# Kernel tuning notes

Measured on AMD Instinct MI355X. Metric: run time of the kernel, lower is better.

## Reference

```python
import jax, jax.numpy as jnp
import numpy as np

HIDDEN = 1024
HEADS = 16
HEAD_DIM = HIDDEN // HEADS
MAX_SEQ = 2048
BATCH = 2
SEQ = 2048


def setup_inputs() -> dict:
    key = jax.random.key(0)
    ks = jax.random.split(key, 6)
    x = jax.random.normal(ks[0], (BATCH, SEQ, HIDDEN), dtype=jnp.float32)
    # torch Linear params expressed as [in, out] weight + bias
    W1 = jax.random.normal(ks[1], (HIDDEN, 4 * HIDDEN), dtype=jnp.float32) * (HIDDEN ** -0.5)
    b1 = jnp.zeros((4 * HIDDEN,), dtype=jnp.float32)
    W2 = jax.random.normal(ks[2], (HIDDEN, HIDDEN), dtype=jnp.float32) * (HIDDEN ** -0.5)
    b2 = jnp.zeros((HIDDEN,), dtype=jnp.float32)
    rel_table = jax.random.normal(ks[3], (2 * MAX_SEQ - 1, HEADS), dtype=jnp.float32) * 0.02
    # causal mask [B, S, S]; True = keep
    attn_mask = jnp.broadcast_to(jnp.tril(jnp.ones((SEQ, SEQ), dtype=bool)), (BATCH, SEQ, SEQ))
    return {"x": x, "W1": W1, "b1": b1, "W2": W2, "b2": b2,
            "rel_table": rel_table, "attn_mask": attn_mask}


def reference(x, W1, b1, W2, b2, rel_table, attn_mask):
    B, S, H = x.shape
    # fused projection + SiLU, then chunk into U, Q, K, V
    activated = jax.nn.silu(jnp.einsum('bsh,hf->bsf', x, W1) + b1)
    U, Qp, Kp, Vp = jnp.split(activated, 4, axis=-1)
    # [B, nH, S, hd]
    def heads(t):
        return t.reshape(B, S, HEADS, HEAD_DIM).transpose(0, 2, 1, 3)
    Q, K, V = heads(Qp), heads(Kp), heads(Vp)
    scale = HEAD_DIM ** -0.5
    scores = jnp.einsum('bnqd,bnkd->bnqk', Q, K) * scale
    # relative position bias gather: idx[i,j] = i - j + MAX_SEQ - 1
    pos = jnp.arange(S)
    rel_idx = pos[:, None] - pos[None, :] + (MAX_SEQ - 1)  # [S, S]
    rel_bias = rel_table[rel_idx].transpose(2, 0, 1)[None]  # [1, nH, S, S]
    scores = scores + rel_bias
    attn = jax.nn.silu(scores)
    attn = jnp.where(attn_mask[:, None, :, :], attn, 0.0)
    out = jnp.einsum('bnqk,bnkd->bnqd', attn, V)
    out = out.transpose(0, 2, 1, 3).reshape(B, S, H)
    gated = out * U
    return jnp.einsum('bsh,hf->bsf', gated, W2) + b2
```

## Files before the change

### kernel.cpp

```cpp
#include <hip/hip_runtime.h>
#include <hip/hip_bf16.h>
#include <math.h>

#define HIDDEN   1024
#define HEADS    16
#define HEAD_DIM 64
#define SEQ      2048
#define BATCH    2
#define FDIM     4096
#define MTOT     4096
#define MAXSEQ   2048

typedef __bf16 bf16x8 __attribute__((ext_vector_type(8)));
typedef float  f32x4  __attribute__((ext_vector_type(4)));
typedef unsigned short u16;

__device__ __forceinline__ float silu_fast(float v) {
    return v * __builtin_amdgcn_rcpf(1.f + __expf(-v));
}

__device__ __forceinline__ u16 f2bf(float f) {
    union { float f; unsigned u; } v; v.f = f;
    unsigned r = v.u + 0x7FFFu + ((v.u >> 16) & 1u);
    return (u16)(r >> 16);
}
__device__ __forceinline__ float bf2f(u16 b) {
    union { unsigned u; float f; } v; v.u = ((unsigned)b) << 16;
    return v.f;
}
__device__ __forceinline__ unsigned pk2(float a, float b) {
    union { __hip_bfloat162 h; unsigned u; } z;
    z.h = __float22bfloat162_rn(make_float2(a, b));
    return z.u;
}

__device__ __forceinline__ void gload16(const void* g, void* l) {
    __builtin_amdgcn_global_load_lds(
        (const __attribute__((address_space(1))) void*)g,
        (__attribute__((address_space(3))) void*)l, 16, 0, 0);
}

__global__ __launch_bounds__(256) void prep_kernel(
    const float* __restrict__ X, const float* __restrict__ W1,
    const float* __restrict__ W2,
    u16* __restrict__ Xb, u16* __restrict__ W1t, u16* __restrict__ W2t,
    unsigned* __restrict__ ticket)
{
    __shared__ u16 T[64][72];
    const int tid = threadIdx.x;
    const int bid = blockIdx.x;

    if (bid == 0 && tid == 0) *ticket = 0u;

    if (bid < 2048) {
        int idx = (bid * 256 + tid) * 8;
        float4 a = *(const float4*)&X[idx];
        float4 b = *(const float4*)&X[idx + 4];
        uint4 pk = make_uint4(pk2(a.x, a.y), pk2(a.z, a.w),
                              pk2(b.x, b.y), pk2(b.z, b.w));
        *(uint4*)&Xb[idx] = pk;
        return;
    }

    const float* W; u16* Wt; int rows, cols, r0, c0;
    if (bid < 3072) {
        int t = bid - 2048;
        W = W1; Wt = W1t; rows = HIDDEN; cols = FDIM;
        c0 = (t & 63) * 64; r0 = (t >> 6) * 64;
    } else {
        int t = bid - 3072;
        W = W2; Wt = W2t; rows = HIDDEN; cols = HIDDEN;
        c0 = (t & 15) * 64; r0 = (t >> 4) * 64;
    }
#pragma unroll
    for (int l = 0; l < 4; ++l) {
        int idx = tid + l * 256;
        int row = idx >> 4;
        int c4  = (idx & 15) * 4;
        float4 v = *(const float4*)&W[(size_t)(r0 + row) * cols + c0 + c4];
        T[c4 + 0][row] = f2bf(v.x);
        T[c4 + 1][row] = f2bf(v.y);
        T[c4 + 2][row] = f2bf(v.z);
        T[c4 + 3][row] = f2bf(v.w);
    }
    __syncthreads();
#pragma unroll
    for (int l = 0; l < 2; ++l) {
        int idx = tid + l * 256;
        int row = idx >> 3;
        int cb  = (idx & 7) * 8;
        *(float4*)&Wt[(size_t)(c0 + row) * rows + r0 + cb] = *(float4*)&T[row][cb];
    }
}

#define GEMM_CORE(A_PTR, BT_PTR, KDIM, BM_, BN_, WMW, WNW)                     \
    enum { MTI = (BM_) / (WMW) / 16, NTI = (BN_) / (WNW) / 16,                 \
           ACH = (BM_) / 8, BCH = (BN_) / 8 };                                 \
    __shared__ __align__(16) u16 As[(BM_) * 64];                               \
    __shared__ __align__(16) u16 Bs[(BN_) * 64];                               \
    const int tid  = threadIdx.x;                                              \
    const int lane = tid & 63;                                                 \
    const int w    = tid >> 6;                                                 \
    const int wm   = w % (WMW), wn = w / (WMW);                                \
    const int l16  = lane & 15, quad = lane >> 4;                              \
    const int m0   = blockIdx.y * (BM_);                                       \
    const int n0   = blockIdx.x * (BN_);                                       \
    const int srow = lane >> 3;                                                \
    const int scol = (((lane & 7) ^ srow)) * 8;     \
    const int xr   = l16 & 7;                           \
    f32x4 acc[MTI][NTI];                                                       \
    _Pragma("unroll")                                                          \
    for (int mt = 0; mt < MTI; ++mt)                                           \
        _Pragma("unroll")                                                      \
        for (int nt = 0; nt < NTI; ++nt)                                       \
            acc[mt][nt] = (f32x4){0.f, 0.f, 0.f, 0.f};                         \
    for (int k0 = 0; k0 < (KDIM); k0 += 64) {                                  \
        __syncthreads();                                                       \
        _Pragma("unroll")                                                      \
        for (int ci = w; ci < ACH; ci += 4) {                                  \
            unsigned off = __builtin_amdgcn_readfirstlane(ci * 1024);          \
            gload16(&(A_PTR)[(size_t)(m0 + ci * 8 + srow) * (KDIM) + k0 + scol],\
                    (char*)As + off);                                          \
        }                                                                      \
        _Pragma("unroll")                                                      \
        for (int ci = w; ci < BCH; ci += 4) {                                  \
            unsigned off = __builtin_amdgcn_readfirstlane(ci * 1024);          \
            gload16(&(BT_PTR)[(size_t)(n0 + ci * 8 + srow) * (KDIM) + k0 + scol],\
                    (char*)Bs + off);                                          \
        }                                                                      \
        __syncthreads();                                                       \
        _Pragma("unroll")                                                      \
        for (int kc = 0; kc < 2; ++kc) {                                       \
            bf16x8 af[MTI], bfr[NTI];                                          \
            const int gsw = ((kc * 4 + quad) ^ xr) * 8;                        \
            _Pragma("unroll")                                                  \
            for (int t = 0; t < MTI; ++t)                                      \
                af[t]  = *(const bf16x8*)&As[(wm * (BM_ / WMW) + t * 16 + l16) \
                                             * 64 + gsw];                      \
            _Pragma("unroll")                                                  \
            for (int t = 0; t < NTI; ++t)                                      \
                bfr[t] = *(const bf16x8*)&Bs[(wn * (BN_ / WNW) + t * 16 + l16) \
                                             * 64 + gsw];                      \
            _Pragma("unroll")                                                  \
            for (int mt = 0; mt < MTI; ++mt)                                   \
                _Pragma("unroll")                                              \
                for (int nt = 0; nt < NTI; ++nt)                               \
                    acc[mt][nt] = __builtin_amdgcn_mfma_f32_16x16x32_bf16(     \
                        bfr[nt], af[mt], acc[mt][nt], 0, 0, 0);                \
        }                                                                      \
    }

__global__ __launch_bounds__(256, 1) void gemm1_mfma_kernel(
    const u16* __restrict__ A, const u16* __restrict__ Bt,
    const float* __restrict__ b1,
    u16* __restrict__ Ub, u16* __restrict__ Qh,
    u16* __restrict__ Kh, u16* __restrict__ Vh)
{
    GEMM_CORE(A, Bt, HIDDEN, 256, 128, 2, 2)

    const int chunk = n0 >> 10;
    u16* dstbase = (chunk == 0) ? Ub : (chunk == 1) ? Qh : (chunk == 2) ? Kh : Vh;
    const float postscale = (chunk == 1) ? 0.125f : 1.0f;

    float4 bias4[NTI]; int nloc[NTI];
#pragma unroll
    for (int nt = 0; nt < NTI; ++nt) {
        int nb = n0 + wn * 64 + nt * 16 + quad * 4;
        bias4[nt] = *(const float4*)&b1[nb];
        nloc[nt] = nb & 1023;
    }
#pragma unroll
    for (int mt = 0; mt < MTI; ++mt) {
        int m  = m0 + wm * 128 + mt * 16 + l16;
        int bb = m >> 11, s = m & 2047;
#pragma unroll
        for (int nt = 0; nt < NTI; ++nt) {
            float v0 = silu_fast(acc[mt][nt][0] + bias4[nt].x) * postscale;
            float v1 = silu_fast(acc[mt][nt][1] + bias4[nt].y) * postscale;
            float v2 = silu_fast(acc[mt][nt][2] + bias4[nt].z) * postscale;
            float v3 = silu_fast(acc[mt][nt][3] + bias4[nt].w) * postscale;
            uint2 pk = make_uint2(pk2(v0, v1), pk2(v2, v3));
            size_t o;
            if (chunk == 0) {
                o = (size_t)m * 1024 + nloc[nt];
            } else {
                int h = nloc[nt] >> 6, d = nloc[nt] & 63;
                o = (size_t)(((bb * HEADS + h) * SEQ) + s) * HEAD_DIM + d;
            }
            *(uint2*)&dstbase[o] = pk;
        }
    }
}

__global__ __launch_bounds__(256) void gemm2_mfma_kernel(
    const u16* __restrict__ A, const u16* __restrict__ Bt,
    const float* __restrict__ b2, float* __restrict__ Out)
{
    GEMM_CORE(A, Bt, HIDDEN, 64, 128, 1, 4)

    float4 bias4[NTI]; int nb[NTI];
#pragma unroll
    for (int nt = 0; nt < NTI; ++nt) {
        nb[nt] = n0 + wn * 32 + nt * 16 + quad * 4;
        bias4[nt] = *(const float4*)&b2[nb[nt]];
    }
#pragma unroll
    for (int mt = 0; mt < MTI; ++mt) {
        int m = m0 + mt * 16 + l16;
#pragma unroll
        for (int nt = 0; nt < NTI; ++nt) {
            float4 vv;
            vv.x = acc[mt][nt][0] + bias4[nt].x;
            vv.y = acc[mt][nt][1] + bias4[nt].y;
            vv.z = acc[mt][nt][2] + bias4[nt].z;
            vv.w = acc[mt][nt][3] + bias4[nt].w;
            *(float4*)&Out[(size_t)m * 1024 + nb[nt]] = vv;
        }
    }
}

__global__ __launch_bounds__(256, 3) void attn_mfma_kernel(
    const u16* __restrict__ Qh, const u16* __restrict__ Kh,
    const u16* __restrict__ Vh, const float* __restrict__ rel,
    const u16* __restrict__ Ub, u16* __restrict__ G,
    unsigned* __restrict__ ticket)
{
    __shared__ u16 Ks[128][72];
    __shared__ u16 Vt[64][136];
    __shared__ u16 Ps[64][72];
    __shared__ float rel_sh[192];
    __shared__ unsigned sh_t;

    const int tid  = threadIdx.x;
    const int lane = tid & 63;
    const int w    = tid >> 6;
    const int quad = lane >> 4;
    const int l16  = lane & 15;

    const int k_r = tid >> 3,       k_c = (tid & 7) * 8;
    const int v_k = (tid & 31) * 2, v_d = (tid >> 5) * 8;
    const int qrow = w * 16 + l16;

    for (;;) {
        if (tid == 0) sh_t = atomicAdd(ticket, 1u);
        __syncthreads();
        const unsigned t = sh_t;
        if (t >= 1024u) return;

        const int qt = 31 - (int)(t >> 5);
        const int bh = (int)(t & 31u);
        const int h  = bh & 15;
        const int bb = bh >> 4;
        const int q0 = qt * 64;

        const u16* Kg = Kh + (size_t)((bb * HEADS + h) * SEQ) * HEAD_DIM;
        const u16* Vg = Vh + (size_t)((bb * HEADS + h) * SEQ) * HEAD_DIM;
        const u16* Qg = Qh + (size_t)((bb * HEADS + h) * SEQ + q0) * HEAD_DIM;

        bf16x8 qa0 = *(const bf16x8*)&Qg[qrow * HEAD_DIM + quad * 8];
        bf16x8 qa1 = *(const bf16x8*)&Qg[qrow * HEAD_DIM + 32 + quad * 8];

        float4 kA0 = *(const float4*)&Kg[(size_t)k_r * 64 + k_c];
        float4 kA1 = *(const float4*)&Kg[(size_t)(k_r + 32) * 64 + k_c];
        float4 vA0 = *(const float4*)&Vg[(size_t)v_k * 64 + v_d];
        float4 vA1 = *(const float4*)&Vg[(size_t)(v_k + 1) * 64 + v_d];
        float4 kB0, kB1, vB0, vB1;
        if (qt >= 1) {
            kB0 = *(const float4*)&Kg[(size_t)(64 + k_r) * 64 + k_c];
            kB1 = *(const float4*)&Kg[(size_t)(64 + k_r + 32) * 64 + k_c];
            vB0 = *(const float4*)&Vg[(size_t)(64 + v_k) * 64 + v_d];
            vB1 = *(const float4*)&Vg[(size_t)(64 + v_k + 1) * 64 + v_d];
        }
        float relreg = 0.f;
        if (tid < 191) relreg = rel[(size_t)(q0 + 1920 + tid) * HEADS + h];

        f32x4 o[4];
#pragma unroll
        for (int dt = 0; dt < 4; ++dt) o[dt] = (f32x4){0.f, 0.f, 0.f, 0.f};

#define ATTN_CHUNK(KOFS, RELOFS, DIAG, QREL)                                   \
    {                                                                          \
        _Pragma("unroll")                                                      \
        for (int ct = 0; ct < 4; ++ct) {                                       \
            bf16x8 ka0 = *(const bf16x8*)&Ks[(KOFS) + ct * 16 + l16][quad * 8];\
            bf16x8 ka1 = *(const bf16x8*)&Ks[(KOFS) + ct * 16 + l16][32 + quad * 8];\
            f32x4 sc = {0.f, 0.f, 0.f, 0.f};                                   \
            sc = __builtin_amdgcn_mfma_f32_16x16x32_bf16(ka0, qa0, sc, 0, 0, 0);\
            sc = __builtin_amdgcn_mfma_f32_16x16x32_bf16(ka1, qa1, sc, 0, 0, 0);\
            const int ib = qrow - ct * 16 - quad * 4 + (RELOFS);               \
            float p[4];                                                        \
            _Pragma("unroll")                                                  \
            for (int r = 0; r < 4; ++r) {                                      \
                float s = sc[r] + rel_sh[ib - r];                              \
                if (DIAG) {                                                    \
                    int kloc = ct * 16 + quad * 4 + r;                         \
                    p[r] = ((QREL) - kloc >= 0) ? silu_fast(s) : 0.f;          \
                } else {                                                       \
                    p[r] = silu_fast(s);                                       \
                }                                                              \
            }                                                                  \
            *(uint2*)&Ps[qrow][ct * 16 + quad * 4] =                           \
                make_uint2(pk2(p[0], p[1]), pk2(p[2], p[3]));                  \
        }                                                                      \
        bf16x8 pa0 = *(const bf16x8*)&Ps[qrow][quad * 8];                      \
        bf16x8 pa1 = *(const bf16x8*)&Ps[qrow][32 + quad * 8];                 \
        const int vo = (KOFS);                                                 \
        _Pragma("unroll")                                                      \
        for (int dt = 0; dt < 4; ++dt) {                                       \
            bf16x8 vb0 = *(const bf16x8*)&Vt[dt * 16 + l16][vo + quad * 8];    \
            bf16x8 vb1 = *(const bf16x8*)&Vt[dt * 16 + l16][vo + 32 + quad * 8];\
            o[dt] = __builtin_amdgcn_mfma_f32_16x16x32_bf16(pa0, vb0, o[dt], 0, 0, 0);\
            o[dt] = __builtin_amdgcn_mfma_f32_16x16x32_bf16(pa1, vb1, o[dt], 0, 0, 0);\
        }                                                                      \
    }

        for (int ip = 0; 2 * ip <= qt; ++ip) {
            const int kp = ip * 128;
            const bool hasB = (2 * ip + 1 <= qt);

            *(float4*)&Ks[k_r][k_c]      = kA0;
            *(float4*)&Ks[k_r + 32][k_c] = kA1;
            {
                union { float4 f; u16 u[8]; } a0, a1;
                a0.f = vA0; a1.f = vA1;
#pragma unroll
                for (int i = 0; i < 8; ++i)
                    *(unsigned*)&Vt[v_d + i][v_k] =
                        (unsigned)a0.u[i] | ((unsigned)a1.u[i] << 16);
            }
            if (hasB) {
                *(float4*)&Ks[64 + k_r][k_c]      = kB0;
                *(float4*)&Ks[64 + k_r + 32][k_c] = kB1;
                union { float4 f; u16 u[8]; } a0, a1;
                a0.f = vB0; a1.f = vB1;
#pragma unroll
                for (int i = 0; i < 8; ++i)
                    *(unsigned*)&Vt[v_d + i][64 + v_k] =
                        (unsigned)a0.u[i] | ((unsigned)a1.u[i] << 16);
            }
            if (tid < 191) rel_sh[tid] = relreg;
            __syncthreads();

            {
                const int nk0 = 2 * ip + 2;
                if (nk0 <= qt) {
                    const int b0 = nk0 * 64;
                    kA0 = *(const float4*)&Kg[(size_t)(b0 + k_r) * 64 + k_c];
                    kA1 = *(const float4*)&Kg[(size_t)(b0 + k_r + 32) * 64 + k_c];
                    vA0 = *(const float4*)&Vg[(size_t)(b0 + v_k) * 64 + v_d];
                    vA1 = *(const float4*)&Vg[(size_t)(b0 + v_k + 1) * 64 + v_d];
                    if (tid < 191)
                        relreg = rel[(size_t)(q0 - kp - 128 + 1920 + tid) * HEADS + h];
                    if (nk0 + 1 <= qt) {
                        const int b1 = b0 + 64;
                        kB0 = *(const float4*)&Kg[(size_t)(b1 + k_r) * 64 + k_c];
                        kB1 = *(const float4*)&Kg[(size_t)(b1 + k_r + 32) * 64 + k_c];
                        vB0 = *(const float4*)&Vg[(size_t)(b1 + v_k) * 64 + v_d];
                        vB1 = *(const float4*)&Vg[(size_t)(b1 + v_k + 1) * 64 + v_d];
                    }
                }
            }

            if (2 * ip == qt) {
                const int qrel0 = q0 - kp + qrow;
                ATTN_CHUNK(0, 127, true, qrel0)
            } else {
                ATTN_CHUNK(0, 127, false, 0)
            }
            if (hasB) {
                if (2 * ip + 1 == qt) {
                    const int qrel1 = q0 - kp - 64 + qrow;
                    ATTN_CHUNK(64, 63, true, qrel1)
                } else {
                    ATTN_CHUNK(64, 63, false, 0)
                }
            }
            __syncthreads();
        }
#undef ATTN_CHUNK

#pragma unroll
        for (int dt = 0; dt < 4; ++dt)
#pragma unroll
            for (int r = 0; r < 4; ++r) {
                int q = q0 + w * 16 + quad * 4 + r;
                size_t base = (size_t)(bb * SEQ + q) * HIDDEN +
                              h * HEAD_DIM + dt * 16 + l16;
                float u = bf2f(Ub[base]);
                G[base] = f2bf(o[dt][r] * u);
            }
    }
}

extern "C" void kernel_launch(void* const* d_in, const int* in_sizes, int n_in,
                              void* d_out, int out_size, void* d_ws, size_t ws_size,
                              hipStream_t stream)
{
    const float* X   = (const float*)d_in[0];
    const float* W1  = (const float*)d_in[1];
    const float* b1  = (const float*)d_in[2];
    const float* W2  = (const float*)d_in[3];
    const float* b2  = (const float*)d_in[4];
    const float* rel = (const float*)d_in[5];
    float* out = (float*)d_out;

    const size_t MH = (size_t)MTOT * HIDDEN;
    u16* Ub   = (u16*)d_ws;
    u16* Qh   = Ub  + MH;
    u16* Kh   = Qh  + MH;
    u16* Vh   = Kh  + MH;
    u16* Gbuf = Vh  + MH;
    u16* Xb   = Gbuf + MH;
    u16* W1t  = Xb  + MH;
    u16* W2t  = W1t + MH;
    unsigned* ticket = (unsigned*)(W2t + (size_t)HIDDEN * HIDDEN);

    prep_kernel<<<3328, 256, 0, stream>>>(X, W1, W2, Xb, W1t, W2t, ticket);
    gemm1_mfma_kernel<<<dim3(FDIM / 128, MTOT / 256), 256, 0, stream>>>(
        Xb, W1t, b1, Ub, Qh, Kh, Vh);
    attn_mfma_kernel<<<dim3(768), 256, 0, stream>>>(
        Qh, Kh, Vh, rel, Ub, Gbuf, ticket);
    gemm2_mfma_kernel<<<dim3(HIDDEN / 128, MTOT / 64), 256, 0, stream>>>(
        Gbuf, W2t, b2, out);
}
```

Before: 240.7 us.

## Split attention waves across key chunks with two q-subtiles each and LDS reduction

Changes the attention kernel's work split. Each wave now owns 32 query rows (two 16-row subtiles) and one of the two 64-key chunks, instead of 16 rows across both chunks. The K and V fragments read from LDS are reused across both subtiles, which halves LDS fragment reads per MFMA. The P buffer gets an XOR swizzle to avoid bank conflicts. Partial outputs from the two key-chunk halves are combined through LDS at the end, which costs an extra barrier and more accumulator registers. On the diagonal or odd tiles, the waves assigned to the missing chunk sit idle.

```diff
diff --git a/kernel.cpp b/kernel.cpp
--- a/kernel.cpp
+++ b/kernel.cpp
@@ -225,9 +225,9 @@
     const u16* __restrict__ Ub, u16* __restrict__ G,
     unsigned* __restrict__ ticket)
 {
-    __shared__ u16 Ks[128][72];
-    __shared__ u16 Vt[64][136];
-    __shared__ u16 Ps[64][72];
+    __shared__ __align__(16) u16 Ks[128][72];
+    __shared__ __align__(16) u16 Vt[64][136];
+    __shared__ __align__(16) u16 Ps[2][64][64];
     __shared__ float rel_sh[192];
     __shared__ unsigned sh_t;
 
@@ -236,10 +236,13 @@
     const int w    = tid >> 6;
     const int quad = lane >> 4;
     const int l16  = lane & 15;
+    const int ws   = w & 1;
+    const int pp   = w >> 1;
+    const int qbase = ws * 32;
+    const int xk   = l16 & 7;
 
     const int k_r = tid >> 3,       k_c = (tid & 7) * 8;
     const int v_k = (tid & 31) * 2, v_d = (tid >> 5) * 8;
-    const int qrow = w * 16 + l16;
 
     for (;;) {
         if (tid == 0) sh_t = atomicAdd(ticket, 1u);
@@ -257,8 +260,13 @@
         const u16* Vg = Vh + (size_t)((bb * HEADS + h) * SEQ) * HEAD_DIM;
         const u16* Qg = Qh + (size_t)((bb * HEADS + h) * SEQ + q0) * HEAD_DIM;
 
-        bf16x8 qa0 = *(const bf16x8*)&Qg[qrow * HEAD_DIM + quad * 8];
-        bf16x8 qa1 = *(const bf16x8*)&Qg[qrow * HEAD_DIM + 32 + quad * 8];
+        bf16x8 qa[2][2];
+#pragma unroll
+        for (int sub = 0; sub < 2; ++sub) {
+            const int qr = qbase + sub * 16 + l16;
+            qa[sub][0] = *(const bf16x8*)&Qg[qr * HEAD_DIM + quad * 8];
+            qa[sub][1] = *(const bf16x8*)&Qg[qr * HEAD_DIM + 32 + quad * 8];
+        }
 
         float4 kA0 = *(const float4*)&Kg[(size_t)k_r * 64 + k_c];
         float4 kA1 = *(const float4*)&Kg[(size_t)(k_r + 32) * 64 + k_c];
@@ -274,45 +282,11 @@
         float relreg = 0.f;
         if (tid < 191) relreg = rel[(size_t)(q0 + 1920 + tid) * HEADS + h];
 
-        f32x4 o[4];
-#pragma unroll
-        for (int dt = 0; dt < 4; ++dt) o[dt] = (f32x4){0.f, 0.f, 0.f, 0.f};
-
-#define ATTN_CHUNK(KOFS, RELOFS, DIAG, QREL)                                   \
-    {                                                                          \
-        _Pragma("unroll")                                                      \
-        for (int ct = 0; ct < 4; ++ct) {                                       \
-            bf16x8 ka0 = *(const bf16x8*)&Ks[(KOFS) + ct * 16 + l16][quad * 8];\
-            bf16x8 ka1 = *(const bf16x8*)&Ks[(KOFS) + ct * 16 + l16][32 + quad * 8];\
-            f32x4 sc = {0.f, 0.f, 0.f, 0.f};                                   \
-            sc = __builtin_amdgcn_mfma_f32_16x16x32_bf16(ka0, qa0, sc, 0, 0, 0);\
-            sc = __builtin_amdgcn_mfma_f32_16x16x32_bf16(ka1, qa1, sc, 0, 0, 0);\
-            const int ib = qrow - ct * 16 - quad * 4 + (RELOFS);               \
-            float p[4];                                                        \
-            _Pragma("unroll")                                                  \
-            for (int r = 0; r < 4; ++r) {                                      \
-                float s = sc[r] + rel_sh[ib - r];                              \
-                if (DIAG) {                                                    \
-                    int kloc = ct * 16 + quad * 4 + r;                         \
-                    p[r] = ((QREL) - kloc >= 0) ? silu_fast(s) : 0.f;          \
-                } else {                                                       \
-                    p[r] = silu_fast(s);                                       \
-                }                                                              \
-            }                                                                  \
-            *(uint2*)&Ps[qrow][ct * 16 + quad * 4] =                           \
-                make_uint2(pk2(p[0], p[1]), pk2(p[2], p[3]));                  \
-        }                                                                      \
-        bf16x8 pa0 = *(const bf16x8*)&Ps[qrow][quad * 8];                      \
-        bf16x8 pa1 = *(const bf16x8*)&Ps[qrow][32 + quad * 8];                 \
-        const int vo = (KOFS);                                                 \
-        _Pragma("unroll")                                                      \
-        for (int dt = 0; dt < 4; ++dt) {                                       \
-            bf16x8 vb0 = *(const bf16x8*)&Vt[dt * 16 + l16][vo + quad * 8];    \
-            bf16x8 vb1 = *(const bf16x8*)&Vt[dt * 16 + l16][vo + 32 + quad * 8];\
-            o[dt] = __builtin_amdgcn_mfma_f32_16x16x32_bf16(pa0, vb0, o[dt], 0, 0, 0);\
-            o[dt] = __builtin_amdgcn_mfma_f32_16x16x32_bf16(pa1, vb1, o[dt], 0, 0, 0);\
-        }                                                                      \
-    }
+        f32x4 o[2][4];
+#pragma unroll
+        for (int sub = 0; sub < 2; ++sub)
+#pragma unroll
+            for (int dt = 0; dt < 4; ++dt) o[sub][dt] = (f32x4){0.f, 0.f, 0.f, 0.f};
 
         for (int ip = 0; 2 * ip <= qt; ++ip) {
             const int kp = ip * 128;
@@ -361,34 +335,93 @@
                 }
             }
 
-            if (2 * ip == qt) {
-                const int qrel0 = q0 - kp + qrow;
-                ATTN_CHUNK(0, 127, true, qrel0)
-            } else {
-                ATTN_CHUNK(0, 127, false, 0)
-            }
-            if (hasB) {
-                if (2 * ip + 1 == qt) {
-                    const int qrel1 = q0 - kp - 64 + qrow;
-                    ATTN_CHUNK(64, 63, true, qrel1)
-                } else {
-                    ATTN_CHUNK(64, 63, false, 0)
+            const int myc = 2 * ip + pp;
+            if (myc <= qt) {
+                const int ko      = pp * 64;
+                const int relofs  = pp ? 63 : 127;
+                const bool diag   = (myc == qt);
+                const int qrelb   = q0 - kp - ko;
+
+#pragma unroll
+                for (int ct = 0; ct < 4; ++ct) {
+                    bf16x8 ka0 = *(const bf16x8*)&Ks[ko + ct * 16 + l16][quad * 8];
+                    bf16x8 ka1 = *(const bf16x8*)&Ks[ko + ct * 16 + l16][32 + quad * 8];
+#pragma unroll
+                    for (int sub = 0; sub < 2; ++sub) {
+                        f32x4 sc = {0.f, 0.f, 0.f, 0.f};
+                        sc = __builtin_amdgcn_mfma_f32_16x16x32_bf16(ka0, qa[sub][0], sc, 0, 0, 0);
+                        sc = __builtin_amdgcn_mfma_f32_16x16x32_bf16(ka1, qa[sub][1], sc, 0, 0, 0);
+                        const int qrow = qbase + sub * 16 + l16;
+                        const int ib   = qrow - ct * 16 - quad * 4 + relofs;
+                        float p4[4];
+                        if (diag) {
+#pragma unroll
+                            for (int r = 0; r < 4; ++r) {
+                                float s = sc[r] + rel_sh[ib - r];
+                                int kloc = ct * 16 + quad * 4 + r;
+                                p4[r] = (qrelb + qrow - kloc >= 0) ? silu_fast(s) : 0.f;
+                            }
+                        } else {
+#pragma unroll
+                            for (int r = 0; r < 4; ++r) {
+                                float s = sc[r] + rel_sh[ib - r];
+                                p4[r] = silu_fast(s);
+                            }
+                        }
+                        const int col = (((2 * ct + (quad >> 1)) ^ xk) << 3) + (quad & 1) * 4;
+                        *(uint2*)&Ps[pp][qrow][col] =
+                            make_uint2(pk2(p4[0], p4[1]), pk2(p4[2], p4[3]));
+                    }
+                }
+
+                bf16x8 pa0[2], pa1[2];
+#pragma unroll
+                for (int sub = 0; sub < 2; ++sub) {
+                    const int qrow = qbase + sub * 16 + l16;
+                    pa0[sub] = *(const bf16x8*)&Ps[pp][qrow][(quad ^ xk) * 8];
+                    pa1[sub] = *(const bf16x8*)&Ps[pp][qrow][((4 + quad) ^ xk) * 8];
+                }
+#pragma unroll
+                for (int dt = 0; dt < 4; ++dt) {
+                    bf16x8 vb0 = *(const bf16x8*)&Vt[dt * 16 + l16][ko + quad * 8];
+                    bf16x8 vb1 = *(const bf16x8*)&Vt[dt * 16 + l16][ko + 32 + quad * 8];
+#pragma unroll
+                    for (int sub = 0; sub < 2; ++sub) {
+                        o[sub][dt] = __builtin_amdgcn_mfma_f32_16x16x32_bf16(pa0[sub], vb0, o[sub][dt], 0, 0, 0);
+                        o[sub][dt] = __builtin_amdgcn_mfma_f32_16x16x32_bf16(pa1[sub], vb1, o[sub][dt], 0, 0, 0);
+                    }
                 }
             }
             __syncthreads();
         }
-#undef ATTN_CHUNK
-
-#pragma unroll
-        for (int dt = 0; dt < 4; ++dt)
-#pragma unroll
-            for (int r = 0; r < 4; ++r) {
-                int q = q0 + w * 16 + quad * 4 + r;
-                size_t base = (size_t)(bb * SEQ + q) * HIDDEN +
-                              h * HEAD_DIM + dt * 16 + l16;
-                float u = bf2f(Ub[base]);
-                G[base] = f2bf(o[dt][r] * u);
-            }
+
+        float* Ored = (float*)&Ks[0][0];
+        if (pp == 1) {
+#pragma unroll
+            for (int sub = 0; sub < 2; ++sub)
+#pragma unroll
+                for (int dt = 0; dt < 4; ++dt)
+                    *(f32x4*)&Ored[((ws << 3) + (sub << 2) + dt) * 256 + lane * 4] =
+                        o[sub][dt];
+        }
+        __syncthreads();
+        if (pp == 0) {
+#pragma unroll
+            for (int sub = 0; sub < 2; ++sub)
+#pragma unroll
+                for (int dt = 0; dt < 4; ++dt) {
+                    f32x4 r4 = *(const f32x4*)&Ored[((ws << 3) + (sub << 2) + dt) * 256 + lane * 4];
+                    o[sub][dt] += r4;
+#pragma unroll
+                    for (int r = 0; r < 4; ++r) {
+                        int q = q0 + qbase + sub * 16 + quad * 4 + r;
+                        size_t base = (size_t)(bb * SEQ + q) * HIDDEN +
+                                      h * HEAD_DIM + dt * 16 + l16;
+                        float u = bf2f(Ub[base]);
+                        G[base] = f2bf(o[sub][dt][r] * u);
+                    }
+                }
+        }
     }
 }
 
```

New measurement: 246.5 us. 1.02x slower.
